# Kernel optimization log

Hardware: AMD Instinct MI355X
Metric: run time of the kernel (lower is better)

## Reference

```python
import jax, jax.numpy as jnp
import numpy as np

L = 4        # num_hidden_layers
D = 1024     # dmodel (== inputsize)
FF = 4096    # dff
H = 16       # num_heads
DH = D // H  # head dim
B, S = 2, 2048
EPS = 1e-6


def _layer_norm(x, g, b):
    m = jnp.mean(x, axis=-1, keepdims=True)
    v = jnp.mean(jnp.square(x - m), axis=-1, keepdims=True)
    return (x - m) * jax.lax.rsqrt(v + EPS) * g + b


def setup_inputs() -> dict:
    key = jax.random.key(0)
    ks = jax.random.split(key, 16)
    sd = 0.02
    inp = {
        "hidden_states": jax.random.normal(ks[0], (B, S, D), jnp.float32),
        # stacked per-layer params (weights stored [in, out])
        "Wq": jax.random.normal(ks[1], (L, D, D), jnp.float32) * sd,
        "bq": jnp.zeros((L, D), jnp.float32),
        "Wk": jax.random.normal(ks[2], (L, D, D), jnp.float32) * sd,
        "bk": jnp.zeros((L, D), jnp.float32),
        "Wv": jax.random.normal(ks[3], (L, D, D), jnp.float32) * sd,
        "bv": jnp.zeros((L, D), jnp.float32),
        "Wp": jax.random.normal(ks[4], (L, D, D), jnp.float32) * sd,
        "bp": jnp.zeros((L, D), jnp.float32),
        "ln1_g": jnp.ones((L, D), jnp.float32),
        "ln1_b": jnp.zeros((L, D), jnp.float32),
        "W1": jax.random.normal(ks[5], (L, D, FF), jnp.float32) * sd,
        "b1": jnp.zeros((L, FF), jnp.float32),
        "W2": jax.random.normal(ks[6], (L, FF, D), jnp.float32) * sd,
        "b2": jnp.zeros((L, D), jnp.float32),
        "ln2_g": jnp.ones((L, D), jnp.float32),
        "ln2_b": jnp.zeros((L, D), jnp.float32),
    }
    return inp


def reference(hidden_states, Wq, bq, Wk, bk, Wv, bv, Wp, bp, ln1_g, ln1_b,
              W1, b1, W2, b2, ln2_g, ln2_b):
    x = hidden_states
    scale = 1.0 / jnp.sqrt(jnp.asarray(DH, x.dtype))
    for l in range(L):
        # --- AttentionIn ---
        q = (x @ Wq[l] + bq[l]).reshape(B, S, H, DH)
        k = (x @ Wk[l] + bk[l]).reshape(B, S, H, DH)
        v = (x @ Wv[l] + bv[l]).reshape(B, S, H, DH)
        scores = jnp.einsum('bqhd,bkhd->bhqk', q, k) * scale
        probs = jax.nn.softmax(scores, axis=-1)
        ctx = jnp.einsum('bhqk,bkhd->bqhd', probs, v).reshape(B, S, D)
        ctx = ctx @ Wp[l] + bp[l]
        x = _layer_norm(ctx + x, ln1_g[l], ln1_b[l])
        # --- AttentionOutput (FFN with residual + LN); dropout=0 ---
        h = jax.nn.relu(x @ W1[l] + b1[l]) @ W2[l] + b2[l]
        x = _layer_norm(h + x, ln2_g[l], ln2_b[l])
    return x
```

## Files before the change

### kernel.cpp

```cpp
#include <hip/hip_runtime.h>

#define D_  1024
#define FF_ 4096
#define H_  16
#define DH_ 64
#define B_  2
#define S_  2048
#define M_  4096

typedef __attribute__((ext_vector_type(8))) __bf16 bf16x8;
typedef __attribute__((ext_vector_type(4))) short short4v;
typedef __attribute__((ext_vector_type(4))) float floatx4;

typedef __attribute__((address_space(1))) unsigned int as1_uint;
typedef __attribute__((address_space(3))) unsigned int as3_uint;

__device__ __forceinline__ unsigned short f2bf(float f) {
    unsigned u = __float_as_uint(f);
    u += 0x7FFFu + ((u >> 16) & 1u);
    return (unsigned short)(u >> 16);
}

__device__ __forceinline__ int packbf(float a, float b) {
    return (int)((__float_as_uint(a) >> 16) | (__float_as_uint(b) & 0xFFFF0000u));
}

__device__ __forceinline__ void gl_lds16(const void* g, void* l) {
    __builtin_amdgcn_global_load_lds((as1_uint*)(unsigned long long)g,
                                     (as3_uint*)l, 16, 0, 0);
}

__global__ __launch_bounds__(256) void transpose_cvt(
    const float* __restrict__ src, unsigned short* __restrict__ dst, int K, int N)
{
    __shared__ float tile[32][33];
    const int tx = threadIdx.x, ty = threadIdx.y;
    const int n0 = blockIdx.x * 32, k0 = blockIdx.y * 32;
#pragma unroll
    for (int i = 0; i < 32; i += 8)
        tile[ty + i][tx] = src[(size_t)(k0 + ty + i) * N + n0 + tx];
    __syncthreads();
#pragma unroll
    for (int i = 0; i < 32; i += 8)
        dst[(size_t)(n0 + ty + i) * K + k0 + tx] = f2bf(tile[tx][ty + i]);
}

__global__ __launch_bounds__(256) void transpose_v(
    const unsigned short* __restrict__ V, unsigned short* __restrict__ VT)
{
    __shared__ unsigned short t[64][72];
    const int bh = blockIdx.y, s0 = blockIdx.x * 64;
    const int tid = threadIdx.x;
#pragma unroll
    for (int i = 0; i < 2; i++) {
        int u = tid + i * 256;
        int s = u >> 3, dc = u & 7;
        uint4 v = *(const uint4*)(V + ((size_t)bh * S_ + s0 + s) * DH_ + dc * 8);
        *(uint4*)&t[s][dc * 8] = v;
    }
    __syncthreads();
    const int dh = tid >> 2, sc = (tid & 3) * 16;
    unsigned v[16];
#pragma unroll
    for (int j = 0; j < 16; j++) v[j] = t[sc + j][dh];
    uint4 o0, o1;
    o0.x = v[0] | (v[1] << 16);  o0.y = v[2] | (v[3] << 16);
    o0.z = v[4] | (v[5] << 16);  o0.w = v[6] | (v[7] << 16);
    o1.x = v[8] | (v[9] << 16);  o1.y = v[10] | (v[11] << 16);
    o1.z = v[12] | (v[13] << 16); o1.w = v[14] | (v[15] << 16);
    unsigned short* dst = VT + ((size_t)bh * DH_ + dh) * S_ + s0 + sc;
    *(uint4*)dst = o0;
    *(uint4*)(dst + 8) = o1;
}

__global__ __launch_bounds__(256) void cvt_x0(
    const float* __restrict__ in, float* __restrict__ xf, unsigned short* __restrict__ xh)
{
    int i = blockIdx.x * 256 + threadIdx.x;
    float4 v = ((const float4*)in)[i];
    ((float4*)xf)[i] = v;
    uint2 h;
    h.x = (unsigned)f2bf(v.x) | ((unsigned)f2bf(v.y) << 16);
    h.y = (unsigned)f2bf(v.z) | ((unsigned)f2bf(v.w) << 16);
    ((uint2*)xh)[i] = h;
}

template <int EPI>
__global__ __launch_bounds__(256) void gemm_bt(
    const unsigned short* __restrict__ A, const unsigned short* __restrict__ BT,
    int M, int N, int K,
    const float* __restrict__ b0, const float* __restrict__ b1, const float* __restrict__ b2,
    float* __restrict__ outF, unsigned short* __restrict__ outH,
    unsigned short* __restrict__ qO, unsigned short* __restrict__ kO, unsigned short* __restrict__ vO)
{
    __shared__ __align__(16) unsigned short As[128 * 32];
    __shared__ __align__(16) unsigned short Bs[128 * 32];

    const int tid = threadIdx.x;
    const int m0 = blockIdx.y * 128, n0 = blockIdx.x * 128;
    const int lane = tid & 63, wv = tid >> 6;
    const int wm = wv & 1, wn = wv >> 1;
    const int cl = lane & 15, quad = lane >> 4;

    const int r0 = tid >> 2, kc0 = (tid & 3) * 8;
    const unsigned short* ga0 = A  + (size_t)(m0 + r0)      * K + kc0;
    const unsigned short* ga1 = A  + (size_t)(m0 + r0 + 64) * K + kc0;
    const unsigned short* gb0 = BT + (size_t)(n0 + r0)      * K + kc0;
    const unsigned short* gb1 = BT + (size_t)(n0 + r0 + 64) * K + kc0;
    unsigned short* lA0 = &As[(size_t)tid * 8];
    unsigned short* lA1 = &As[(size_t)(tid + 256) * 8];
    unsigned short* lB0 = &Bs[(size_t)tid * 8];
    unsigned short* lB1 = &Bs[(size_t)(tid + 256) * 8];

    floatx4 acc[4][4];
#pragma unroll
    for (int i = 0; i < 4; i++)
#pragma unroll
        for (int j = 0; j < 4; j++) acc[i][j] = (floatx4){0.f, 0.f, 0.f, 0.f};

    for (int kt = 0; kt < K; kt += 32) {
        gl_lds16(ga0 + kt, lA0);
        gl_lds16(ga1 + kt, lA1);
        gl_lds16(gb0 + kt, lB0);
        gl_lds16(gb1 + kt, lB1);
        __syncthreads();

        bf16x8 av[4], bv[4];
#pragma unroll
        for (int mi = 0; mi < 4; mi++)
            av[mi] = *(const bf16x8*)&As[(wm * 64 + mi * 16 + cl) * 32 + quad * 8];
#pragma unroll
        for (int ni = 0; ni < 4; ni++)
            bv[ni] = *(const bf16x8*)&Bs[(wn * 64 + ni * 16 + cl) * 32 + quad * 8];
#pragma unroll
        for (int mi = 0; mi < 4; mi++)
#pragma unroll
            for (int ni = 0; ni < 4; ni++)
                acc[mi][ni] = __builtin_amdgcn_mfma_f32_16x16x32_bf16(
                    av[mi], bv[ni], acc[mi][ni], 0, 0, 0);
        __syncthreads();
    }

#pragma unroll
    for (int mi = 0; mi < 4; mi++) {
#pragma unroll
        for (int ni = 0; ni < 4; ni++) {
            const int c = n0 + wn * 64 + ni * 16 + cl;
#pragma unroll
            for (int r = 0; r < 4; r++) {
                const int rr = m0 + wm * 64 + mi * 16 + quad * 4 + r;
                float v = acc[mi][ni][r];
                if (EPI == 0) {
                    outF[(size_t)rr * N + c] = v + b0[c];
                } else if (EPI == 1) {
                    float t = v + b0[c];
                    outH[(size_t)rr * N + c] = f2bf(t > 0.f ? t : 0.f);
                } else {
                    const int kind = c >> 10, cc = c & 1023;
                    const float* bp = (kind == 0) ? b0 : (kind == 1) ? b1 : b2;
                    float t = v + bp[cc];
                    if (kind == 0) t *= 0.18033688f;
                    const int h = cc >> 6, dh = cc & 63;
                    const int bb = rr >> 11, s = rr & 2047;
                    unsigned short* dst = (kind == 0) ? qO : (kind == 1) ? kO : vO;
                    dst[((size_t)(bb * H_ + h) * S_ + s) * DH_ + dh] = f2bf(t);
                }
            }
        }
    }
}

__global__ __launch_bounds__(256) void gemm_bt64(
    const unsigned short* __restrict__ A, const unsigned short* __restrict__ BT,
    int M, int N, int K, const float* __restrict__ bias, float* __restrict__ outF)
{
    __shared__ __align__(16) unsigned short As[64 * 32];
    __shared__ __align__(16) unsigned short Bs[128 * 32];

    const int tid = threadIdx.x;
    const int m0 = blockIdx.y * 64, n0 = blockIdx.x * 128;
    const int lane = tid & 63, wv = tid >> 6;
    const int wm = wv & 1, wn = wv >> 1;
    const int cl = lane & 15, quad = lane >> 4;

    const int r0 = tid >> 2, kc0 = (tid & 3) * 8;
    const unsigned short* ga  = A  + (size_t)(m0 + r0)      * K + kc0;
    const unsigned short* gb0 = BT + (size_t)(n0 + r0)      * K + kc0;
    const unsigned short* gb1 = BT + (size_t)(n0 + r0 + 64) * K + kc0;
    unsigned short* lA  = &As[(size_t)tid * 8];
    unsigned short* lB0 = &Bs[(size_t)tid * 8];
    unsigned short* lB1 = &Bs[(size_t)(tid + 256) * 8];

    floatx4 acc[2][4];
#pragma unroll
    for (int i = 0; i < 2; i++)
#pragma unroll
        for (int j = 0; j < 4; j++) acc[i][j] = (floatx4){0.f, 0.f, 0.f, 0.f};

    for (int kt = 0; kt < K; kt += 32) {
        gl_lds16(ga + kt, lA);
        gl_lds16(gb0 + kt, lB0);
        gl_lds16(gb1 + kt, lB1);
        __syncthreads();

        bf16x8 av[2], bv[4];
#pragma unroll
        for (int mi = 0; mi < 2; mi++)
            av[mi] = *(const bf16x8*)&As[(wm * 32 + mi * 16 + cl) * 32 + quad * 8];
#pragma unroll
        for (int ni = 0; ni < 4; ni++)
            bv[ni] = *(const bf16x8*)&Bs[(wn * 64 + ni * 16 + cl) * 32 + quad * 8];
#pragma unroll
        for (int mi = 0; mi < 2; mi++)
#pragma unroll
            for (int ni = 0; ni < 4; ni++)
                acc[mi][ni] = __builtin_amdgcn_mfma_f32_16x16x32_bf16(
                    av[mi], bv[ni], acc[mi][ni], 0, 0, 0);
        __syncthreads();
    }

#pragma unroll
    for (int mi = 0; mi < 2; mi++)
#pragma unroll
        for (int ni = 0; ni < 4; ni++) {
            const int c = n0 + wn * 64 + ni * 16 + cl;
#pragma unroll
            for (int r = 0; r < 4; r++) {
                const int rr = m0 + wm * 32 + mi * 16 + quad * 4 + r;
                outF[(size_t)rr * N + c] = acc[mi][ni][r] + bias[c];
            }
        }
}

__global__ __launch_bounds__(256) void attn_kernel(
    const unsigned short* __restrict__ Qg, const unsigned short* __restrict__ Kg,
    const unsigned short* __restrict__ VTg, unsigned short* __restrict__ ctx)
{
    __shared__ __align__(16) unsigned short Ks[64 * 64];
    __shared__ __align__(16) unsigned short Vs[64 * 64];

    const int tid = threadIdx.x, lane = tid & 63, wv = tid >> 6;
    const int cl = lane & 15, quad = lane >> 4;

    const int lin = blockIdx.x;
    const int idx = lin >> 3;
    const int bh  = (lin & 7) * 4 + (idx & 3);
    const int qt  = idx >> 2;
    const int qrow = qt * 64 + wv * 16 + cl;
    const size_t bhS = (size_t)bh * S_;

    bf16x8 aq[2];
#pragma unroll
    for (int ks = 0; ks < 2; ks++)
        aq[ks] = *(const bf16x8*)(Qg + (bhS + qrow) * DH_ + ks * 32 + quad * 8);

    floatx4 O[4];
#pragma unroll
    for (int i = 0; i < 4; i++) O[i] = (floatx4){0.f, 0.f, 0.f, 0.f};
    float l_cur = 0.f;

    const int g0 = tid, g1 = tid + 256;
    const int r_0 = g0 >> 3, c_0 = (g0 & 7) ^ (r_0 & 7);
    const int r_1 = g1 >> 3, c_1 = (g1 & 7) ^ (r_1 & 7);
    const unsigned short* kp0 = Kg + (bhS + r_0) * DH_ + c_0 * 8;
    const unsigned short* kp1 = Kg + (bhS + r_1) * DH_ + c_1 * 8;
    const unsigned short* vp0 = VTg + ((size_t)bh * DH_ + r_0) * S_ + c_0 * 8;
    const unsigned short* vp1 = VTg + ((size_t)bh * DH_ + r_1) * S_ + c_1 * 8;
    unsigned short* lk0 = &Ks[(size_t)g0 * 8];
    unsigned short* lk1 = &Ks[(size_t)g1 * 8];
    unsigned short* lv0 = &Vs[(size_t)g0 * 8];
    unsigned short* lv1 = &Vs[(size_t)g1 * 8];

    const unsigned short* krd0[4];
    const unsigned short* krd1[4];
    const unsigned short* vrd[4][4];
#pragma unroll
    for (int mi = 0; mi < 4; mi++) {
        const int row = mi * 16 + cl;
        krd0[mi] = &Ks[(row * 8 + (quad       ^ (cl & 7))) * 8];
        krd1[mi] = &Ks[(row * 8 + ((4 + quad) ^ (cl & 7))) * 8];
#pragma unroll
        for (int c16 = 0; c16 < 4; c16++) {
            const int slot = (c16 * 2 + (quad >> 1)) ^ (cl & 7);
            vrd[c16][mi] = &Vs[(row * 8 + slot) * 8 + (quad & 1) * 4];
        }
    }

    for (int k0 = 0; k0 < S_; k0 += 64) {
        __syncthreads();
        gl_lds16(kp0 + (size_t)k0 * DH_, lk0);
        gl_lds16(kp1 + (size_t)k0 * DH_, lk1);
        gl_lds16(vp0 + k0, lv0);
        gl_lds16(vp1 + k0, lv1);
        __syncthreads();

        floatx4 sc[4];
#pragma unroll
        for (int mi = 0; mi < 4; mi++) {
            bf16x8 kf0 = *(const bf16x8*)krd0[mi];
            bf16x8 kf1 = *(const bf16x8*)krd1[mi];
            floatx4 z = (floatx4){0.f, 0.f, 0.f, 0.f};
            z = __builtin_amdgcn_mfma_f32_16x16x32_bf16(kf0, aq[0], z, 0, 0, 0);
            sc[mi] = __builtin_amdgcn_mfma_f32_16x16x32_bf16(kf1, aq[1], z, 0, 0, 0);
        }

        int pk[4][2];
#pragma unroll
        for (int mi = 0; mi < 4; mi++) {
            float p0 = __builtin_amdgcn_exp2f(sc[mi][0]);
            float p1 = __builtin_amdgcn_exp2f(sc[mi][1]);
            float p2 = __builtin_amdgcn_exp2f(sc[mi][2]);
            float p3 = __builtin_amdgcn_exp2f(sc[mi][3]);
            l_cur += (p0 + p1) + (p2 + p3);
            pk[mi][0] = packbf(p0, p1);
            pk[mi][1] = packbf(p2, p3);
        }

#pragma unroll
        for (int c16 = 0; c16 < 4; c16++) {
            union { int i[2]; short4v s; } pb;
            pb.i[0] = pk[c16][0];
            pb.i[1] = pk[c16][1];
#pragma unroll
            for (int mi2 = 0; mi2 < 4; mi2++) {
                short4v va = *(const short4v*)vrd[c16][mi2];
                O[mi2] = __builtin_amdgcn_mfma_f32_16x16x16bf16_1k(va, pb.s, O[mi2], 0, 0, 0);
            }
        }
    }

    l_cur += __shfl_xor(l_cur, 16);
    l_cur += __shfl_xor(l_cur, 32);

    const float invl = 1.f / l_cur;
    const int b = bh >> 4, h = bh & 15;
    unsigned short* cp = ctx + ((size_t)(b * S_ + qrow)) * D_ + h * DH_ + quad * 4;
#pragma unroll
    for (int mi2 = 0; mi2 < 4; mi2++) {
        unsigned short w[4];
#pragma unroll
        for (int r = 0; r < 4; r++) w[r] = f2bf(O[mi2][r] * invl);
        unsigned o0 = (unsigned)w[0] | ((unsigned)w[1] << 16);
        unsigned o1 = (unsigned)w[2] | ((unsigned)w[3] << 16);
        uint2 ov; ov.x = o0; ov.y = o1;
        *(uint2*)(cp + mi2 * 16) = ov;
    }
}

__global__ __launch_bounds__(256) void ln_kernel(
    const float* __restrict__ t, const float* __restrict__ xr,
    const float* __restrict__ g, const float* __restrict__ b,
    float* __restrict__ xf, unsigned short* __restrict__ xh, float* __restrict__ extra)
{
    const int row = blockIdx.x, tid = threadIdx.x;
    const float4 a = ((const float4*)(t  + (size_t)row * D_))[tid];
    const float4 c = ((const float4*)(xr + (size_t)row * D_))[tid];
    float4 y;
    y.x = a.x + c.x; y.y = a.y + c.y; y.z = a.z + c.z; y.w = a.w + c.w;
    float s  = y.x + y.y + y.z + y.w;
    float sq = y.x * y.x + y.y * y.y + y.z * y.z + y.w * y.w;
#pragma unroll
    for (int off = 1; off < 64; off <<= 1) {
        s  += __shfl_xor(s, off);
        sq += __shfl_xor(sq, off);
    }
    __shared__ float red[8];
    const int wv = tid >> 6, lane = tid & 63;
    if (lane == 0) { red[wv] = s; red[4 + wv] = sq; }
    __syncthreads();
    s  = red[0] + red[1] + red[2] + red[3];
    sq = red[4] + red[5] + red[6] + red[7];
    const float mean = s * (1.f / D_);
    const float var  = sq * (1.f / D_) - mean * mean;
    const float ri   = rsqrtf(var + 1e-6f);
    const float4 gg = ((const float4*)g)[tid];
    const float4 bb = ((const float4*)b)[tid];
    float4 o;
    o.x = (y.x - mean) * ri * gg.x + bb.x;
    o.y = (y.y - mean) * ri * gg.y + bb.y;
    o.z = (y.z - mean) * ri * gg.z + bb.z;
    o.w = (y.w - mean) * ri * gg.w + bb.w;
    ((float4*)(xf + (size_t)row * D_))[tid] = o;
    uint2 h;
    h.x = (unsigned)f2bf(o.x) | ((unsigned)f2bf(o.y) << 16);
    h.y = (unsigned)f2bf(o.z) | ((unsigned)f2bf(o.w) << 16);
    ((uint2*)(xh + (size_t)row * D_))[tid] = h;
    if (extra) ((float4*)(extra + (size_t)row * D_))[tid] = o;
}

extern "C" void kernel_launch(void* const* d_in, const int* in_sizes, int n_in,
                              void* d_out, int out_size, void* d_ws, size_t ws_size,
                              hipStream_t stream)
{
    const float* hs  = (const float*)d_in[0];
    const float* Wq  = (const float*)d_in[1];
    const float* bq  = (const float*)d_in[2];
    const float* Wk  = (const float*)d_in[3];
    const float* bk  = (const float*)d_in[4];
    const float* Wv  = (const float*)d_in[5];
    const float* bv  = (const float*)d_in[6];
    const float* Wp  = (const float*)d_in[7];
    const float* bp  = (const float*)d_in[8];
    const float* g1  = (const float*)d_in[9];
    const float* be1 = (const float*)d_in[10];
    const float* W1  = (const float*)d_in[11];
    const float* b1  = (const float*)d_in[12];
    const float* W2  = (const float*)d_in[13];
    const float* b2  = (const float*)d_in[14];
    const float* g2  = (const float*)d_in[15];
    const float* be2 = (const float*)d_in[16];

    char* w = (char*)d_ws;
    auto alloc = [&](size_t bytes) { char* p = w; w += (bytes + 255) & ~(size_t)255; return p; };
    unsigned short* wqkvT = (unsigned short*)alloc(3072ull * 1024 * 2);
    unsigned short* wpT   = (unsigned short*)alloc(1024ull * 1024 * 2);
    unsigned short* w1T   = (unsigned short*)alloc(4096ull * 1024 * 2);
    unsigned short* w2T   = (unsigned short*)alloc(1024ull * 4096 * 2);
    float*          xf    = (float*)alloc(4096ull * 1024 * 4);
    unsigned short* xh    = (unsigned short*)alloc(4096ull * 1024 * 2);
    unsigned short* qb_   = (unsigned short*)alloc(4096ull * 1024 * 2);
    unsigned short* kb_   = (unsigned short*)alloc(4096ull * 1024 * 2);
    unsigned short* vb_   = (unsigned short*)alloc(4096ull * 1024 * 2);
    unsigned short* ctx   = (unsigned short*)alloc(4096ull * 1024 * 2);
    float*          tf    = (float*)alloc(4096ull * 1024 * 4);
    unsigned short* hh    = (unsigned short*)alloc(4096ull * 4096 * 2);
    unsigned short* vtb   = hh;

    const dim3 blk(256);
    const dim3 tb(32, 8);

    cvt_x0<<<4096, blk, 0, stream>>>(hs, xf, xh);

    for (int l = 0; l < 4; l++) {
        transpose_cvt<<<dim3(32, 32),  tb, 0, stream>>>(Wq + (size_t)l * D_ * D_,  wqkvT,                 D_, D_);
        transpose_cvt<<<dim3(32, 32),  tb, 0, stream>>>(Wk + (size_t)l * D_ * D_,  wqkvT + 1024 * 1024,   D_, D_);
        transpose_cvt<<<dim3(32, 32),  tb, 0, stream>>>(Wv + (size_t)l * D_ * D_,  wqkvT + 2 * 1024 * 1024, D_, D_);
        transpose_cvt<<<dim3(32, 32),  tb, 0, stream>>>(Wp + (size_t)l * D_ * D_,  wpT, D_, D_);
        transpose_cvt<<<dim3(128, 32), tb, 0, stream>>>(W1 + (size_t)l * D_ * FF_, w1T, D_, FF_);
        transpose_cvt<<<dim3(32, 128), tb, 0, stream>>>(W2 + (size_t)l * FF_ * D_, w2T, FF_, D_);

        gemm_bt<2><<<dim3(24, 32), blk, 0, stream>>>(xh, wqkvT, M_, 3 * D_, D_,
            bq + l * D_, bk + l * D_, bv + l * D_,
            nullptr, nullptr, qb_, kb_, vb_);

        transpose_v<<<dim3(32, 32), blk, 0, stream>>>(vb_, vtb);

        attn_kernel<<<1024, blk, 0, stream>>>(qb_, kb_, vtb, ctx);

        gemm_bt64<<<dim3(8, 64), blk, 0, stream>>>(ctx, wpT, M_, D_, D_,
            bp + l * D_, tf);

        ln_kernel<<<4096, blk, 0, stream>>>(tf, xf, g1 + l * D_, be1 + l * D_, xf, xh, nullptr);

        gemm_bt<1><<<dim3(32, 32), blk, 0, stream>>>(xh, w1T, M_, FF_, D_,
            b1 + l * FF_, nullptr, nullptr, nullptr, hh, nullptr, nullptr, nullptr);

        gemm_bt64<<<dim3(8, 64), blk, 0, stream>>>(hh, w2T, M_, D_, FF_,
            b2 + l * D_, tf);

        ln_kernel<<<4096, blk, 0, stream>>>(tf, xf, g2 + l * D_, be2 + l * D_, xf, xh,
            (l == 3) ? (float*)d_out : nullptr);
    }
}
```

Baseline: 1.358 ms.

## Use 64-wide K tiles with XOR-swizzled LDS and split-K for N=1024 GEMMs

The 128x128 GEMM now stages 64-wide K slices in LDS with an XOR swizzle, which halves the barriers per K and avoids LDS bank conflicts. The separate 64-row GEMM for the projection and FFN2 is replaced by the 128x128 kernel with a split-K of two. Each split writes its own fp32 partial buffer, and the bias add and partial reduction move into the layernorm kernel. This aims to give better MFMA utilisation and occupancy for the N=1024 GEMMs, at the cost of extra fp32 partial traffic and double the LDS per block.

```diff
diff --git a/kernel.cpp b/kernel.cpp
--- a/kernel.cpp
+++ b/kernel.cpp
@@ -85,32 +85,29 @@
     ((uint2*)xh)[i] = h;
 }
 
-template <int EPI>
-__global__ __launch_bounds__(256) void gemm_bt(
+template <int EPI, int KSPLIT>
+__global__ __launch_bounds__(256) void gemm128(
     const unsigned short* __restrict__ A, const unsigned short* __restrict__ BT,
     int M, int N, int K,
     const float* __restrict__ b0, const float* __restrict__ b1, const float* __restrict__ b2,
     float* __restrict__ outF, unsigned short* __restrict__ outH,
     unsigned short* __restrict__ qO, unsigned short* __restrict__ kO, unsigned short* __restrict__ vO)
 {
-    __shared__ __align__(16) unsigned short As[128 * 32];
-    __shared__ __align__(16) unsigned short Bs[128 * 32];
+    __shared__ __align__(16) unsigned short As[128 * 64];
+    __shared__ __align__(16) unsigned short Bs[128 * 64];
 
     const int tid = threadIdx.x;
     const int m0 = blockIdx.y * 128, n0 = blockIdx.x * 128;
+    const int kchunk = K / KSPLIT;
+    const int kbase = (KSPLIT > 1) ? (int)blockIdx.z * kchunk : 0;
     const int lane = tid & 63, wv = tid >> 6;
     const int wm = wv & 1, wn = wv >> 1;
     const int cl = lane & 15, quad = lane >> 4;
 
-    const int r0 = tid >> 2, kc0 = (tid & 3) * 8;
-    const unsigned short* ga0 = A  + (size_t)(m0 + r0)      * K + kc0;
-    const unsigned short* ga1 = A  + (size_t)(m0 + r0 + 64) * K + kc0;
-    const unsigned short* gb0 = BT + (size_t)(n0 + r0)      * K + kc0;
-    const unsigned short* gb1 = BT + (size_t)(n0 + r0 + 64) * K + kc0;
-    unsigned short* lA0 = &As[(size_t)tid * 8];
-    unsigned short* lA1 = &As[(size_t)(tid + 256) * 8];
-    unsigned short* lB0 = &Bs[(size_t)tid * 8];
-    unsigned short* lB1 = &Bs[(size_t)(tid + 256) * 8];
+    const int srow = tid >> 3, sslot = tid & 7;
+    const int schk = sslot ^ (srow & 7);
+    const unsigned short* gA = A  + (size_t)(m0 + srow) * K + kbase + schk * 8;
+    const unsigned short* gB = BT + (size_t)(n0 + srow) * K + kbase + schk * 8;
 
     floatx4 acc[4][4];
 #pragma unroll
@@ -118,29 +115,42 @@
 #pragma unroll
         for (int j = 0; j < 4; j++) acc[i][j] = (floatx4){0.f, 0.f, 0.f, 0.f};
 
-    for (int kt = 0; kt < K; kt += 32) {
-        gl_lds16(ga0 + kt, lA0);
-        gl_lds16(ga1 + kt, lA1);
-        gl_lds16(gb0 + kt, lB0);
-        gl_lds16(gb1 + kt, lB1);
+    for (int kt = 0; kt < kchunk; kt += 64) {
+#pragma unroll
+        for (int i = 0; i < 4; i++) {
+            gl_lds16(gA + (size_t)(32 * i) * K + kt, &As[(size_t)(tid + 256 * i) * 8]);
+            gl_lds16(gB + (size_t)(32 * i) * K + kt, &Bs[(size_t)(tid + 256 * i) * 8]);
+        }
         __syncthreads();
 
-        bf16x8 av[4], bv[4];
+        bf16x8 av[4][2], bv[4][2];
+#pragma unroll
+        for (int mi = 0; mi < 4; mi++) {
+            const int row = wm * 64 + mi * 16 + cl;
+#pragma unroll
+            for (int ks = 0; ks < 2; ks++)
+                av[mi][ks] = *(const bf16x8*)&As[row * 64 + (((ks * 4 + quad) ^ (cl & 7)) * 8)];
+        }
+#pragma unroll
+        for (int ni = 0; ni < 4; ni++) {
+            const int row = wn * 64 + ni * 16 + cl;
+#pragma unroll
+            for (int ks = 0; ks < 2; ks++)
+                bv[ni][ks] = *(const bf16x8*)&Bs[row * 64 + (((ks * 4 + quad) ^ (cl & 7)) * 8)];
+        }
 #pragma unroll
         for (int mi = 0; mi < 4; mi++)
-            av[mi] = *(const bf16x8*)&As[(wm * 64 + mi * 16 + cl) * 32 + quad * 8];
-#pragma unroll
-        for (int ni = 0; ni < 4; ni++)
-            bv[ni] = *(const bf16x8*)&Bs[(wn * 64 + ni * 16 + cl) * 32 + quad * 8];
-#pragma unroll
-        for (int mi = 0; mi < 4; mi++)
-#pragma unroll
-            for (int ni = 0; ni < 4; ni++)
+#pragma unroll
+            for (int ni = 0; ni < 4; ni++) {
                 acc[mi][ni] = __builtin_amdgcn_mfma_f32_16x16x32_bf16(
-                    av[mi], bv[ni], acc[mi][ni], 0, 0, 0);
+                    av[mi][0], bv[ni][0], acc[mi][ni], 0, 0, 0);
+                acc[mi][ni] = __builtin_amdgcn_mfma_f32_16x16x32_bf16(
+                    av[mi][1], bv[ni][1], acc[mi][ni], 0, 0, 0);
+            }
         __syncthreads();
     }
 
+    float* outFz = (EPI == 0) ? outF + (size_t)blockIdx.z * M * N : outF;
 #pragma unroll
     for (int mi = 0; mi < 4; mi++) {
 #pragma unroll
@@ -151,7 +161,7 @@
                 const int rr = m0 + wm * 64 + mi * 16 + quad * 4 + r;
                 float v = acc[mi][ni][r];
                 if (EPI == 0) {
-                    outF[(size_t)rr * N + c] = v + b0[c];
+                    outFz[(size_t)rr * N + c] = v;
                 } else if (EPI == 1) {
                     float t = v + b0[c];
                     outH[(size_t)rr * N + c] = f2bf(t > 0.f ? t : 0.f);
@@ -170,68 +180,6 @@
     }
 }
 
-__global__ __launch_bounds__(256) void gemm_bt64(
-    const unsigned short* __restrict__ A, const unsigned short* __restrict__ BT,
-    int M, int N, int K, const float* __restrict__ bias, float* __restrict__ outF)
-{
-    __shared__ __align__(16) unsigned short As[64 * 32];
-    __shared__ __align__(16) unsigned short Bs[128 * 32];
-
-    const int tid = threadIdx.x;
-    const int m0 = blockIdx.y * 64, n0 = blockIdx.x * 128;
-    const int lane = tid & 63, wv = tid >> 6;
-    const int wm = wv & 1, wn = wv >> 1;
-    const int cl = lane & 15, quad = lane >> 4;
-
-    const int r0 = tid >> 2, kc0 = (tid & 3) * 8;
-    const unsigned short* ga  = A  + (size_t)(m0 + r0)      * K + kc0;
-    const unsigned short* gb0 = BT + (size_t)(n0 + r0)      * K + kc0;
-    const unsigned short* gb1 = BT + (size_t)(n0 + r0 + 64) * K + kc0;
-    unsigned short* lA  = &As[(size_t)tid * 8];
-    unsigned short* lB0 = &Bs[(size_t)tid * 8];
-    unsigned short* lB1 = &Bs[(size_t)(tid + 256) * 8];
-
-    floatx4 acc[2][4];
-#pragma unroll
-    for (int i = 0; i < 2; i++)
-#pragma unroll
-        for (int j = 0; j < 4; j++) acc[i][j] = (floatx4){0.f, 0.f, 0.f, 0.f};
-
-    for (int kt = 0; kt < K; kt += 32) {
-        gl_lds16(ga + kt, lA);
-        gl_lds16(gb0 + kt, lB0);
-        gl_lds16(gb1 + kt, lB1);
-        __syncthreads();
-
-        bf16x8 av[2], bv[4];
-#pragma unroll
-        for (int mi = 0; mi < 2; mi++)
-            av[mi] = *(const bf16x8*)&As[(wm * 32 + mi * 16 + cl) * 32 + quad * 8];
-#pragma unroll
-        for (int ni = 0; ni < 4; ni++)
-            bv[ni] = *(const bf16x8*)&Bs[(wn * 64 + ni * 16 + cl) * 32 + quad * 8];
-#pragma unroll
-        for (int mi = 0; mi < 2; mi++)
-#pragma unroll
-            for (int ni = 0; ni < 4; ni++)
-                acc[mi][ni] = __builtin_amdgcn_mfma_f32_16x16x32_bf16(
-                    av[mi], bv[ni], acc[mi][ni], 0, 0, 0);
-        __syncthreads();
-    }
-
-#pragma unroll
-    for (int mi = 0; mi < 2; mi++)
-#pragma unroll
-        for (int ni = 0; ni < 4; ni++) {
-            const int c = n0 + wn * 64 + ni * 16 + cl;
-#pragma unroll
-            for (int r = 0; r < 4; r++) {
-                const int rr = m0 + wm * 32 + mi * 16 + quad * 4 + r;
-                outF[(size_t)rr * N + c] = acc[mi][ni][r] + bias[c];
-            }
-        }
-}
-
 __global__ __launch_bounds__(256) void attn_kernel(
     const unsigned short* __restrict__ Qg, const unsigned short* __restrict__ Kg,
     const unsigned short* __restrict__ VTg, unsigned short* __restrict__ ctx)
@@ -347,16 +295,25 @@
     }
 }
 
+template <int NP>
 __global__ __launch_bounds__(256) void ln_kernel(
-    const float* __restrict__ t, const float* __restrict__ xr,
+    const float* __restrict__ t, const float* __restrict__ bias,
+    const float* __restrict__ xr,
     const float* __restrict__ g, const float* __restrict__ b,
     float* __restrict__ xf, unsigned short* __restrict__ xh, float* __restrict__ extra)
 {
     const int row = blockIdx.x, tid = threadIdx.x;
-    const float4 a = ((const float4*)(t  + (size_t)row * D_))[tid];
+    float4 a = ((const float4*)(t + (size_t)row * D_))[tid];
+#pragma unroll
+    for (int p = 1; p < NP; p++) {
+        const float4 ap = ((const float4*)(t + (size_t)p * M_ * D_ + (size_t)row * D_))[tid];
+        a.x += ap.x; a.y += ap.y; a.z += ap.z; a.w += ap.w;
+    }
+    const float4 bs = ((const float4*)bias)[tid];
     const float4 c = ((const float4*)(xr + (size_t)row * D_))[tid];
     float4 y;
-    y.x = a.x + c.x; y.y = a.y + c.y; y.z = a.z + c.z; y.w = a.w + c.w;
+    y.x = a.x + bs.x + c.x; y.y = a.y + bs.y + c.y;
+    y.z = a.z + bs.z + c.z; y.w = a.w + bs.w + c.w;
     float s  = y.x + y.y + y.z + y.w;
     float sq = y.x * y.x + y.y * y.y + y.z * y.z + y.w * y.w;
 #pragma unroll
@@ -422,7 +379,7 @@
     unsigned short* kb_   = (unsigned short*)alloc(4096ull * 1024 * 2);
     unsigned short* vb_   = (unsigned short*)alloc(4096ull * 1024 * 2);
     unsigned short* ctx   = (unsigned short*)alloc(4096ull * 1024 * 2);
-    float*          tf    = (float*)alloc(4096ull * 1024 * 4);
+    float*          part  = (float*)alloc(2ull * 4096 * 1024 * 4);
     unsigned short* hh    = (unsigned short*)alloc(4096ull * 4096 * 2);
     unsigned short* vtb   = hh;
 
@@ -439,7 +396,7 @@
         transpose_cvt<<<dim3(128, 32), tb, 0, stream>>>(W1 + (size_t)l * D_ * FF_, w1T, D_, FF_);
         transpose_cvt<<<dim3(32, 128), tb, 0, stream>>>(W2 + (size_t)l * FF_ * D_, w2T, FF_, D_);
 
-        gemm_bt<2><<<dim3(24, 32), blk, 0, stream>>>(xh, wqkvT, M_, 3 * D_, D_,
+        gemm128<2, 1><<<dim3(24, 32), blk, 0, stream>>>(xh, wqkvT, M_, 3 * D_, D_,
             bq + l * D_, bk + l * D_, bv + l * D_,
             nullptr, nullptr, qb_, kb_, vb_);
 
@@ -447,18 +404,20 @@
 
         attn_kernel<<<1024, blk, 0, stream>>>(qb_, kb_, vtb, ctx);
 
-        gemm_bt64<<<dim3(8, 64), blk, 0, stream>>>(ctx, wpT, M_, D_, D_,
-            bp + l * D_, tf);
-
-        ln_kernel<<<4096, blk, 0, stream>>>(tf, xf, g1 + l * D_, be1 + l * D_, xf, xh, nullptr);
-
-        gemm_bt<1><<<dim3(32, 32), blk, 0, stream>>>(xh, w1T, M_, FF_, D_,
+        gemm128<0, 2><<<dim3(8, 32, 2), blk, 0, stream>>>(ctx, wpT, M_, D_, D_,
+            nullptr, nullptr, nullptr, part, nullptr, nullptr, nullptr, nullptr);
+
+        ln_kernel<2><<<4096, blk, 0, stream>>>(part, bp + l * D_, xf,
+            g1 + l * D_, be1 + l * D_, xf, xh, nullptr);
+
+        gemm128<1, 1><<<dim3(32, 32), blk, 0, stream>>>(xh, w1T, M_, FF_, D_,
             b1 + l * FF_, nullptr, nullptr, nullptr, hh, nullptr, nullptr, nullptr);
 
-        gemm_bt64<<<dim3(8, 64), blk, 0, stream>>>(hh, w2T, M_, D_, FF_,
-            b2 + l * D_, tf);
-
-        ln_kernel<<<4096, blk, 0, stream>>>(tf, xf, g2 + l * D_, be2 + l * D_, xf, xh,
+        gemm128<0, 2><<<dim3(8, 32, 2), blk, 0, stream>>>(hh, w2T, M_, D_, FF_,
+            nullptr, nullptr, nullptr, part, nullptr, nullptr, nullptr, nullptr);
+
+        ln_kernel<2><<<4096, blk, 0, stream>>>(part, b2 + l * D_, xf,
+            g2 + l * D_, be2 + l * D_, xf, xh,
             (l == 3) ? (float*)d_out : nullptr);
     }
 }
```

Result: faster. 1.195 ms (-12.0%).
